# Kernel tuning notes

Measured on AMD Instinct MI355X. Metric: run time of the kernel, lower is better.

The kernel has to match this reference:

```python
import math
import jax, jax.numpy as jnp
import numpy as np

INV_SQRT2 = 1.0 / math.sqrt(2.0)
TOPK = 8


def _interleave(a, b):
    # a, b: [B, T2, F] -> [B, 2*T2, F] with a at even, b at odd time indices
    B, T2, F = a.shape
    return jnp.stack([a, b], axis=2).reshape(B, 2 * T2, F)


def setup_inputs() -> dict:
    key = jax.random.key(0)
    x = jax.random.normal(key, (8, 8192, 512), dtype=jnp.float32)
    return {"x": x}


def reference(x):
    B, T, F = x.shape  # T assumed even (setup guarantees it; torch pads otherwise)
    x_even = x[:, 0::2, :]
    x_odd = x[:, 1::2, :]
    x_low = (x_even + x_odd) * INV_SQRT2   # [B, T/2, F]
    x_high = (x_even - x_odd) * INV_SQRT2  # [B, T/2, F]

    T2 = T // 2
    k = min(TOPK, T2)
    # top-k by |x_high| along time axis, per (batch, feature) column
    mag = jnp.abs(x_high).transpose(0, 2, 1)          # [B, F, T2]
    _, idx = jax.lax.top_k(mag, k)                    # [B, F, k]
    mask = jnp.zeros((B, F, T2), dtype=bool)
    mask = mask.at[jnp.arange(B)[:, None, None],
                   jnp.arange(F)[None, :, None], idx].set(True)
    mask = mask.transpose(0, 2, 1)                    # [B, T2, F]
    xh_sparse = jnp.where(mask, x_high, jnp.zeros_like(x_high))

    low_half = x_low * INV_SQRT2
    high_half = xh_sparse * INV_SQRT2
    main = _interleave(low_half, low_half)            # even: +low, odd: -0 => same
    detail_sparse = _interleave(high_half, -high_half)
    return main, detail_sparse
```

## Files before the change

kernel.cpp:

```cpp
#include <hip/hip_runtime.h>
#include <math.h>

#define B_  8
#define T_  8192
#define T2_ 4096
#define F_  512
#define F4_ 128
#define K_  8

typedef unsigned long long u64;
typedef float fvec4 __attribute__((ext_vector_type(4)));

__device__ __forceinline__ void ins8(u64 (&a)[K_], u64 k) {
    if (k <= a[K_ - 1]) return;
#pragma unroll
    for (int j = 0; j < K_; ++j) {
        u64 hi = (k > a[j]) ? k : a[j];
        u64 lo = (k > a[j]) ? a[j] : k;
        a[j] = hi;
        k = lo;
    }
}

__global__ __launch_bounds__(256) void haar_phase1(
    const fvec4* __restrict__ x4, fvec4* __restrict__ mainOut,
    u64* __restrict__ cand, int S, int L)
{
    const int tx   = threadIdx.x;
    const int f4   = blockIdx.x * 64 + tx;
    const int slot = blockIdx.y * 4 + threadIdx.y;
    const int b    = blockIdx.z;
    const int t2_0 = slot * L;

    u64 a0[K_], a1[K_], a2[K_], a3[K_];
#pragma unroll
    for (int j = 0; j < K_; ++j) { a0[j] = 0; a1[j] = 0; a2[j] = 0; a3[j] = 0; }

    const size_t rowBase = (size_t)b * T_;

    for (int t = 0; t < L; ++t) {
        const int t2 = t2_0 + t;
        const size_t re = (rowBase + 2 * (size_t)t2) * F4_ + f4;
        fvec4 e = x4[re];
        fvec4 o = x4[re + F4_];
        fvec4 low = (e + o) * 0.5f;
        __builtin_nontemporal_store(low, &mainOut[re]);
        __builtin_nontemporal_store(low, &mainOut[re + F4_]);
        const u64 it = (u64)(unsigned)(~t2);
        ins8(a0, ((u64)__float_as_uint(fabsf(e.x - o.x)) << 32) | it);
        ins8(a1, ((u64)__float_as_uint(fabsf(e.y - o.y)) << 32) | it);
        ins8(a2, ((u64)__float_as_uint(fabsf(e.z - o.z)) << 32) | it);
        ins8(a3, ((u64)__float_as_uint(fabsf(e.w - o.w)) << 32) | it);
    }

    const size_t colBase = (size_t)b * F_ + 4 * (size_t)f4;
    u64* d0 = cand + ((colBase + 0) * S + slot) * K_;
    u64* d1 = cand + ((colBase + 1) * S + slot) * K_;
    u64* d2 = cand + ((colBase + 2) * S + slot) * K_;
    u64* d3 = cand + ((colBase + 3) * S + slot) * K_;
#pragma unroll
    for (int j = 0; j < K_; ++j) { d0[j] = a0[j]; d1[j] = a1[j]; d2[j] = a2[j]; d3[j] = a3[j]; }
}

__global__ __launch_bounds__(256) void haar_phase2(
    const float* __restrict__ x, const u64* __restrict__ cand,
    float* __restrict__ out, int S)
{
    const int lane = threadIdx.x & 63;
    const int wv   = threadIdx.x >> 6;
    const int col  = blockIdx.x * 4 + wv;
    const int b    = col >> 9;
    const int f    = col & (F_ - 1);
    const int n    = S * K_;

    const u64* c = cand + (size_t)col * n;
    u64 a[K_];
#pragma unroll
    for (int j = 0; j < K_; ++j) a[j] = 0;
    for (int e = lane; e < n; e += 64) ins8(a, c[e]);

    u64 wkey = 0;
#pragma unroll
    for (int j = 0; j < K_; ++j) {
        u64 m = a[0];
#pragma unroll
        for (int s = 32; s > 0; s >>= 1) {
            u64 t = __shfl_xor(m, s, 64);
            m = (t > m) ? t : m;
        }
        if (a[0] == m) {
#pragma unroll
            for (int q = 0; q < K_ - 1; ++q) a[q] = a[q + 1];
            a[K_ - 1] = 0;
        }
        if (lane == j) wkey = m;
    }

    float* det = out + (size_t)B_ * T_ * F_;
    if (lane < K_) {
        const int t2 = (int)(~(unsigned)wkey);
        const size_t re = ((size_t)b * T_ + 2 * (size_t)t2) * F_ + f;
        const float e = x[re];
        const float o = x[re + F_];
        const float v = (e - o) * 0.5f;
        det[re]      = v;
        det[re + F_] = -v;
    }
}

extern "C" void kernel_launch(void* const* d_in, const int* in_sizes, int n_in,
                              void* d_out, int out_size, void* d_ws, size_t ws_size,
                              hipStream_t stream) {
    const float* x = (const float*)d_in[0];
    float* out = (float*)d_out;
    float* detail = out + (size_t)B_ * T_ * F_;

    hipMemsetAsync(detail, 0, (size_t)B_ * T_ * F_ * sizeof(float), stream);

    int S = 128;
    while (S > 32 && (size_t)B_ * F_ * (size_t)S * K_ * sizeof(u64) > ws_size) S >>= 1;
    const int L = T2_ / S;
    u64* cand = (u64*)d_ws;

    dim3 gA(F4_ / 64, S / 4, B_);
    dim3 bA(64, 4, 1);
    hipLaunchKernelGGL(haar_phase1, gA, bA, 0, stream,
                       (const fvec4*)x, (fvec4*)out, cand, S, L);

    const int nb = (B_ * F_) / 4;
    hipLaunchKernelGGL(haar_phase2, dim3(nb), dim3(256), 0, stream,
                       x, cand, out, S);
}
```

Baseline: 390.3 us.

## Fuse detail zero-fill into phase1 and narrow per-thread columns to two

Removes the separate hipMemsetAsync of the detail output and has phase1 write zeros to the detail buffer alongside the main output, which saves one launch. Each thread now handles two feature columns (float2) instead of four, cutting per-thread top-k register state in half and doubling the number of threads. Phase1 also gets an unroll of 2. The trade-off is narrower 8-byte memory accesses instead of 16-byte ones. Correctness relies on phase2 running after phase1 so its sparse detail writes land on top of the zeros.

Result: slower. 398.3 us (+2.1%).

```diff
diff --git a/kernel.cpp b/kernel.cpp
--- a/kernel.cpp
+++ b/kernel.cpp
@@ -5,11 +5,11 @@
 #define T_  8192
 #define T2_ 4096
 #define F_  512
-#define F4_ 128
+#define F2_ 256
 #define K_  8
 
 typedef unsigned long long u64;
-typedef float fvec4 __attribute__((ext_vector_type(4)));
+typedef float fvec2 __attribute__((ext_vector_type(2)));
 
 __device__ __forceinline__ void ins8(u64 (&a)[K_], u64 k) {
     if (k <= a[K_ - 1]) return;
@@ -23,43 +23,43 @@
 }
 
 __global__ __launch_bounds__(256) void haar_phase1(
-    const fvec4* __restrict__ x4, fvec4* __restrict__ mainOut,
-    u64* __restrict__ cand, int S, int L)
+    const fvec2* __restrict__ x2, fvec2* __restrict__ mainOut,
+    fvec2* __restrict__ detOut, u64* __restrict__ cand, int S, int L)
 {
     const int tx   = threadIdx.x;
-    const int f4   = blockIdx.x * 64 + tx;
+    const int f2   = blockIdx.x * 64 + tx;
     const int slot = blockIdx.y * 4 + threadIdx.y;
     const int b    = blockIdx.z;
     const int t2_0 = slot * L;
 
-    u64 a0[K_], a1[K_], a2[K_], a3[K_];
+    u64 a0[K_], a1[K_];
 #pragma unroll
-    for (int j = 0; j < K_; ++j) { a0[j] = 0; a1[j] = 0; a2[j] = 0; a3[j] = 0; }
+    for (int j = 0; j < K_; ++j) { a0[j] = 0; a1[j] = 0; }
 
     const size_t rowBase = (size_t)b * T_;
+    const fvec2 z = (fvec2)0.0f;
 
+#pragma unroll 2
     for (int t = 0; t < L; ++t) {
         const int t2 = t2_0 + t;
-        const size_t re = (rowBase + 2 * (size_t)t2) * F4_ + f4;
-        fvec4 e = x4[re];
-        fvec4 o = x4[re + F4_];
-        fvec4 low = (e + o) * 0.5f;
+        const size_t re = (rowBase + 2 * (size_t)t2) * F2_ + f2;
+        fvec2 e = x2[re];
+        fvec2 o = x2[re + F2_];
+        fvec2 low = (e + o) * 0.5f;
         __builtin_nontemporal_store(low, &mainOut[re]);
-        __builtin_nontemporal_store(low, &mainOut[re + F4_]);
+        __builtin_nontemporal_store(low, &mainOut[re + F2_]);
+        __builtin_nontemporal_store(z, &detOut[re]);
+        __builtin_nontemporal_store(z, &detOut[re + F2_]);
         const u64 it = (u64)(unsigned)(~t2);
         ins8(a0, ((u64)__float_as_uint(fabsf(e.x - o.x)) << 32) | it);
         ins8(a1, ((u64)__float_as_uint(fabsf(e.y - o.y)) << 32) | it);
-        ins8(a2, ((u64)__float_as_uint(fabsf(e.z - o.z)) << 32) | it);
-        ins8(a3, ((u64)__float_as_uint(fabsf(e.w - o.w)) << 32) | it);
     }
 
-    const size_t colBase = (size_t)b * F_ + 4 * (size_t)f4;
+    const size_t colBase = (size_t)b * F_ + 2 * (size_t)f2;
     u64* d0 = cand + ((colBase + 0) * S + slot) * K_;
     u64* d1 = cand + ((colBase + 1) * S + slot) * K_;
-    u64* d2 = cand + ((colBase + 2) * S + slot) * K_;
-    u64* d3 = cand + ((colBase + 3) * S + slot) * K_;
 #pragma unroll
-    for (int j = 0; j < K_; ++j) { d0[j] = a0[j]; d1[j] = a1[j]; d2[j] = a2[j]; d3[j] = a3[j]; }
+    for (int j = 0; j < K_; ++j) { d0[j] = a0[j]; d1[j] = a1[j]; }
 }
 
 __global__ __launch_bounds__(256) void haar_phase2(
@@ -115,17 +115,15 @@
     float* out = (float*)d_out;
     float* detail = out + (size_t)B_ * T_ * F_;
 
-    hipMemsetAsync(detail, 0, (size_t)B_ * T_ * F_ * sizeof(float), stream);
-
     int S = 128;
     while (S > 32 && (size_t)B_ * F_ * (size_t)S * K_ * sizeof(u64) > ws_size) S >>= 1;
     const int L = T2_ / S;
     u64* cand = (u64*)d_ws;
 
-    dim3 gA(F4_ / 64, S / 4, B_);
+    dim3 gA(F2_ / 64, S / 4, B_);
     dim3 bA(64, 4, 1);
     hipLaunchKernelGGL(haar_phase1, gA, bA, 0, stream,
-                       (const fvec4*)x, (fvec4*)out, cand, S, L);
+                       (const fvec2*)x, (fvec2*)out, (fvec2*)detail, cand, S, L);
 
     const int nb = (B_ * F_) / 4;
     hipLaunchKernelGGL(haar_phase2, dim3(nb), dim3(256), 0, stream,
```
